# Optimization experiments

Hardware: AMD Instinct MI355X
Metric: run time of the kernel (lower is better)

## Reference

```python
import jax, jax.numpy as jnp
import numpy as np

N = 50000      # nodes
E = 800000     # edges
D_IN = 128     # raw feature dim
H = 96         # hidden_channels
K = 8          # experts
L = 4          # num_layers
C = 40         # classes


def setup_inputs() -> dict:
    key = jax.random.key(0)
    ks = jax.random.split(key, 10)
    stdv = 1.0 / np.sqrt(H)
    inp = {
        'x': jax.random.normal(ks[0], (N, D_IN), dtype=jnp.float32),
        'edge_index': jax.random.randint(ks[1], (2, E), 0, N, dtype=jnp.int64),
        # fcs[0]: Linear(d, hidden); fcs[1]: Linear(hidden, c)
        'fc0_w': jax.random.normal(ks[2], (D_IN, H), dtype=jnp.float32) * 0.05,
        'fc0_b': jnp.zeros((H,), dtype=jnp.float32),
        'fc1_w': jax.random.normal(ks[3], (H, C), dtype=jnp.float32) * 0.05,
        'fc1_b': jnp.zeros((C,), dtype=jnp.float32),
        # context_enc (method='node'): per-layer Linear(hidden, K)
        'ctx_w': jax.random.normal(ks[4], (L, H, K), dtype=jnp.float32) * 0.05,
        'ctx_b': jnp.zeros((L, K), dtype=jnp.float32),
        # GraphMultiConvolution weights: [L, K, hidden, hidden], uniform(-stdv, stdv)
        'conv_w': jax.random.uniform(ks[5], (L, K, H, H), dtype=jnp.float32,
                                     minval=-stdv, maxval=stdv),
    }
    return inp


def reference(x, edge_index, fc0_w, fc0_b, fc1_w, fc1_b, ctx_w, ctx_b, conv_w):
    # eval-mode forward (training=False): no dropout, softmax routing
    row = edge_index[0]
    col = edge_index[1]
    h = jax.nn.relu(x @ fc0_w + fc0_b)                     # [N, H]
    for i in range(L):
        # routing logits and soft expert weights z: [N, K]
        z = jax.nn.softmax(h @ ctx_w[i] + ctx_b[i], axis=-1)
        # spmm aggregation: hi[r] = sum over edges (r, c) of h[c]
        hi = jax.ops.segment_sum(h[col], row, num_segments=N)  # [N, H]
        # K-expert batched matmul: [N, K, H]
        outs = jnp.einsum('nd,kdo->nko', hi, conv_w[i])
        # gumbel/softmax-weighted combine + residual
        out = jnp.einsum('nk,nko->no', z, outs) + h
        h = jax.nn.relu(out)
    return h @ fc1_w + fc1_b                               # [N, C]
```

## Files before the change

kernel.cpp:

```cpp
#include <hip/hip_runtime.h>

#define N_NODES 50000
#define N_EDGES 800000
#define DIN     128
#define H       96
#define K_EXP   8
#define L_LAYERS 4
#define C_OUT   40

#define GSZ 6250

typedef _Float16 f16;
typedef f16 f16x2 __attribute__((ext_vector_type(2)));
typedef f16 f16x4 __attribute__((ext_vector_type(4)));
typedef f16 f16x8 __attribute__((ext_vector_type(8)));
typedef float f32x4 __attribute__((ext_vector_type(4)));

#define CONV_TOT (L_LAYERS * K_EXP * H * H)
#define FC0_TOT  (DIN * H)
#define FC1_TOT  (48 * H)


__global__ __launch_bounds__(256) void count_convert(const int* __restrict__ row,
                                                     int* __restrict__ deg,
                                                     int* __restrict__ p,
                                                     const float* __restrict__ conv_w,
                                                     const float* __restrict__ fc0_w,
                                                     const float* __restrict__ fc1_w,
                                                     f16* __restrict__ wfrag,
                                                     f16* __restrict__ fc0t,
                                                     f16* __restrict__ fc1t) {
    int i = blockIdx.x * blockDim.x + threadIdx.x;
    if (i < N_EDGES) {
        p[i] = atomicAdd(&deg[row[i]], 1);
        return;
    }
    int j = i - N_EDGES;
    if (j < CONV_TOT) {
        int o = j % H;
        int t = j / H;
        int d = t % H;
        int lk = t / H;
        int ct = o >> 4, lc = o & 15;
        int ks = d >> 5, quad = (d >> 3) & 3, jj = d & 7;
        wfrag[(size_t)lk * 9216 + ct * 1536 + ks * 512 + (quad * 16 + lc) * 8 + jj] =
            (f16)conv_w[j];
    } else if (j < CONV_TOT + FC0_TOT) {
        int q = j - CONV_TOT;
        int o = q % H, d = q / H;
        fc0t[o * DIN + d] = (f16)fc0_w[q];
    } else if (j < CONV_TOT + FC0_TOT + FC1_TOT) {
        int q = j - CONV_TOT - FC0_TOT;
        int o = q / H, d = q % H;
        fc1t[q] = (o < C_OUT) ? (f16)fc1_w[d * C_OUT + o] : (f16)0.f;
    }
}

__global__ __launch_bounds__(1024) void scanA(const int* __restrict__ deg,
                                              int* __restrict__ rowptr,
                                              int* __restrict__ partial, int n) {
    __shared__ int wsum[16];
    int tid  = threadIdx.x;
    int lane = tid & 63, wid = tid >> 6;
    int idx = blockIdx.x * 1024 + tid;
    int v = (idx < n) ? deg[idx] : 0;
    int s = v;
    #pragma unroll
    for (int off = 1; off < 64; off <<= 1) {
        int t = __shfl_up(s, off, 64);
        if (lane >= off) s += t;
    }
    if (lane == 63) wsum[wid] = s;
    __syncthreads();
    if (wid == 0 && lane < 16) {
        int w = wsum[lane];
        #pragma unroll
        for (int off = 1; off < 16; off <<= 1) {
            int t = __shfl_up(w, off, 16);
            if (lane >= off) w += t;
        }
        wsum[lane] = w;
    }
    __syncthreads();
    int waveoff = (wid == 0) ? 0 : wsum[wid - 1];
    if (idx < n) rowptr[idx + 1] = waveoff + s;
    if (tid == 1023) partial[blockIdx.x] = waveoff + s;
}

__global__ __launch_bounds__(1024) void scanC(int* __restrict__ rowptr,
                                              const int* __restrict__ partial,
                                              int nb, int n) {
    __shared__ int boff_s;
    int tid = threadIdx.x;
    if (tid < 64) {
        int v = (tid < nb && tid < (int)blockIdx.x) ? partial[tid] : 0;
        #pragma unroll
        for (int off = 32; off >= 1; off >>= 1) v += __shfl_xor(v, off, 64);
        if (tid == 0) boff_s = v;
    }
    __syncthreads();
    int boff = boff_s;
    int idx = blockIdx.x * 1024 + tid;
    if (idx == 0) rowptr[0] = 0;
    if (idx < n) rowptr[idx + 1] += boff;
}

__global__ __launch_bounds__(256) void scatter_store_xcd(const int* __restrict__ row,
                                                         const int* __restrict__ col,
                                                         const int* __restrict__ p,
                                                         const int* __restrict__ rowptr,
                                                         int* __restrict__ csr, int e) {
    int g = blockIdx.x & 7;
    int rlo = g * GSZ, rhi = rlo + GSZ;
    int stride = (gridDim.x >> 3) * 256;
    for (int i = (blockIdx.x >> 3) * 256 + threadIdx.x; i < e; i += stride) {
        int r = row[i];
        if (r >= rlo && r < rhi)
            csr[rowptr[r] + p[i]] = col[i];
    }
}


#define SPMM_BLOCKS ((N_NODES + 31) / 32)
#define CTX_BLOCKS  ((N_NODES + 255) / 256)

__global__ __launch_bounds__(256) void layer_pre(const f16* __restrict__ h16,
                                                 const int* __restrict__ rowptr,
                                                 const int* __restrict__ csr,
                                                 f16* __restrict__ hi16,
                                                 const float* __restrict__ cw,
                                                 const float* __restrict__ cb,
                                                 float* __restrict__ zt, int n) {
    __shared__ float ws[H * K_EXP];
    __shared__ float bs[K_EXP];
    int tid = threadIdx.x;
    if ((int)blockIdx.x < SPMM_BLOCKS) {
        int r0 = blockIdx.x * 32 + (tid >> 4);
        int r1 = r0 + 16;
        int li = tid & 15;
        if (r0 >= n) return;
        int j0 = rowptr[r0], e0 = rowptr[r0 + 1];
        int j1 = 0, e1 = 0;
        if (r1 < n) { j1 = rowptr[r1]; e1 = rowptr[r1 + 1]; }
        bool act = li < 12;
        float accA[8] = {}, accB[8] = {};
        for (;;) {
            int m0 = e0 - j0; if (m0 > 16) m0 = 16;
            int m1 = e1 - j1; if (m1 > 16) m1 = 16;
            if (m0 <= 0 && m1 <= 0) break;
            int c0 = 0, c1 = 0;
            if (li < m0) c0 = csr[j0 + li];
            if (li < m1) c1 = csr[j1 + li];
            int mm = m0 > m1 ? m0 : m1;
            int t = 0;
            for (; t + 4 <= mm; t += 4) {
                f16x8 vA[4], vB[4];
                bool aA[4], aB[4];
                #pragma unroll
                for (int u = 0; u < 4; u++) {
                    int cc0 = __shfl(c0, t + u, 16);
                    int cc1 = __shfl(c1, t + u, 16);
                    aA[u] = act && (t + u < m0);
                    aB[u] = act && (t + u < m1);
                    vA[u] = f16x8{}; vB[u] = f16x8{};
                    if (aA[u]) vA[u] = *(const f16x8*)(h16 + (size_t)cc0 * H + li * 8);
                    if (aB[u]) vB[u] = *(const f16x8*)(h16 + (size_t)cc1 * H + li * 8);
                }
                #pragma unroll
                for (int u = 0; u < 4; u++) {
                    if (aA[u]) {
                        #pragma unroll
                        for (int q = 0; q < 8; q++) accA[q] += (float)vA[u][q];
                    }
                    if (aB[u]) {
                        #pragma unroll
                        for (int q = 0; q < 8; q++) accB[q] += (float)vB[u][q];
                    }
                }
            }
            for (; t < mm; t++) {
                int cc0 = __shfl(c0, t, 16), cc1 = __shfl(c1, t, 16);
                bool a0 = act && (t < m0), a1 = act && (t < m1);
                f16x8 v0 = {}, v1 = {};
                if (a0) v0 = *(const f16x8*)(h16 + (size_t)cc0 * H + li * 8);
                if (a1) v1 = *(const f16x8*)(h16 + (size_t)cc1 * H + li * 8);
                if (a0) {
                    #pragma unroll
                    for (int q = 0; q < 8; q++) accA[q] += (float)v0[q];
                }
                if (a1) {
                    #pragma unroll
                    for (int q = 0; q < 8; q++) accB[q] += (float)v1[q];
                }
            }
            j0 += m0; j1 += m1;
        }
        if (act) {
            f16x8 oA;
            #pragma unroll
            for (int q = 0; q < 8; q++) oA[q] = (f16)accA[q];
            *(f16x8*)(hi16 + (size_t)r0 * H + li * 8) = oA;
            if (r1 < n) {
                f16x8 oB;
                #pragma unroll
                for (int q = 0; q < 8; q++) oB[q] = (f16)accB[q];
                *(f16x8*)(hi16 + (size_t)r1 * H + li * 8) = oB;
            }
        }
    } else {
        for (int t = tid; t < H * K_EXP; t += 256) ws[t] = cw[t];
        if (tid < K_EXP) bs[tid] = cb[tid];
        __syncthreads();
        int node = ((int)blockIdx.x - SPMM_BLOCKS) * 256 + tid;
        if (node >= n) return;
        float acc[K_EXP];
        #pragma unroll
        for (int k = 0; k < K_EXP; k++) acc[k] = bs[k];
        const f16* hr = h16 + (size_t)node * H;
        #pragma unroll 3
        for (int c8 = 0; c8 < 12; c8++) {
            f16x8 v = *(const f16x8*)(hr + c8 * 8);
            #pragma unroll
            for (int j = 0; j < 8; j++) {
                float hv = (float)v[j];
                int d = c8 * 8 + j;
                #pragma unroll
                for (int k = 0; k < K_EXP; k++) acc[k] += hv * ws[d * K_EXP + k];
            }
        }
        float mx = acc[0];
        #pragma unroll
        for (int k = 1; k < K_EXP; k++) mx = fmaxf(mx, acc[k]);
        float s = 0.f;
        #pragma unroll
        for (int k = 0; k < K_EXP; k++) { acc[k] = __expf(acc[k] - mx); s += acc[k]; }
        float inv = 1.f / s;
        #pragma unroll
        for (int k = 0; k < K_EXP; k++)
            zt[(size_t)k * N_NODES + node] = acc[k] * inv;
    }
}


#define FPAD 136

__global__ __launch_bounds__(256) void fc0_kernel(const float* __restrict__ x,
                                                  const f16* __restrict__ fc0t,
                                                  const float* __restrict__ b,
                                                  f16* __restrict__ h16, int n) {
    __shared__ f16 As[64 * FPAD];
    __shared__ f16 Ws[96 * FPAD];
    int tid = threadIdx.x;
    int l = tid & 63, w = tid >> 6;
    int quad = l >> 4, lc = l & 15;
    int row0 = blockIdx.x * 64;

    for (int t = tid; t < 2048; t += 256) {
        int m = t >> 5, c4 = (t & 31) * 4;
        int gr = row0 + m;
        float4 v = {0.f, 0.f, 0.f, 0.f};
        if (gr < n) v = *(const float4*)(x + (size_t)gr * DIN + c4);
        f16x4 h4 = {(f16)v.x, (f16)v.y, (f16)v.z, (f16)v.w};
        *(f16x4*)&As[m * FPAD + c4] = h4;
    }
    for (int t = tid; t < 1536; t += 256) {
        int o = t >> 4, c8 = (t & 15) * 8;
        *(f16x8*)&Ws[o * FPAD + c8] = *(const f16x8*)(fc0t + o * DIN + c8);
    }
    __syncthreads();

    f16x8 afr[4];
    #pragma unroll
    for (int ks = 0; ks < 4; ks++)
        afr[ks] = *(const f16x8*)&As[(16 * w + lc) * FPAD + ks * 32 + quad * 8];

    f32x4 acc[6] = {};
    #pragma unroll
    for (int ct = 0; ct < 6; ct++) {
        #pragma unroll
        for (int ks = 0; ks < 4; ks++) {
            f16x8 bfr = *(const f16x8*)&Ws[(ct * 16 + lc) * FPAD + ks * 32 + quad * 8];
            acc[ct] = __builtin_amdgcn_mfma_f32_16x16x32_f16(afr[ks], bfr, acc[ct], 0, 0, 0);
        }
    }

    int m0 = 16 * w + quad * 4;
    #pragma unroll
    for (int r = 0; r < 4; r++) {
        int gr = row0 + m0 + r;
        if (gr < n) {
            #pragma unroll
            for (int ct = 0; ct < 6; ct++) {
                int o = ct * 16 + lc;
                h16[(size_t)gr * H + o] = (f16)fmaxf(acc[ct][r] + b[o], 0.f);
            }
        }
    }
}


#define EG_STAGE 2
#define EG_HALFS (EG_STAGE * 9216)

__global__ __launch_bounds__(256) void expert_gemm(const f16* __restrict__ hi16,
                                                   const f16* __restrict__ hin16,
                                                   const f16* __restrict__ wfrag,
                                                   const float* __restrict__ zt,
                                                   f16* __restrict__ hout16, int n) {
    __shared__ f16 Wl[EG_HALFS];
    int tid = threadIdx.x;
    int l = tid & 63, w = tid >> 6;
    int quad = l >> 4, lc = l & 15;
    int wrow0 = blockIdx.x * 64 + w * 16;

    f16x8 afr[3];
    #pragma unroll
    for (int ks = 0; ks < 3; ks++)
        afr[ks] = *(const f16x8*)(hi16 + (size_t)(wrow0 + lc) * H + ks * 32 + quad * 8);

    f32x4 acc[6] = {};

    for (int kb = 0; kb < K_EXP; kb += EG_STAGE) {
        __syncthreads();
        const f16* src = wfrag + (size_t)kb * 9216;
        for (int t = tid; t < EG_HALFS / 8; t += 256)
            *(f16x8*)&Wl[t * 8] = *(const f16x8*)(src + t * 8);
        __syncthreads();

        #pragma unroll
        for (int k2 = 0; k2 < EG_STAGE; k2++) {
            int k = kb + k2;
            f32x4 zf = *(const f32x4*)(zt + (size_t)k * N_NODES + wrow0 + quad * 4);
            #pragma unroll
            for (int ct = 0; ct < 6; ct++) {
                f16x8 b0 = *(const f16x8*)&Wl[k2 * 9216 + ct * 1536 + 0 * 512 + l * 8];
                f16x8 b1 = *(const f16x8*)&Wl[k2 * 9216 + ct * 1536 + 1 * 512 + l * 8];
                f16x8 b2 = *(const f16x8*)&Wl[k2 * 9216 + ct * 1536 + 2 * 512 + l * 8];
                f32x4 tmp = {};
                tmp = __builtin_amdgcn_mfma_f32_16x16x32_f16(afr[0], b0, tmp, 0, 0, 0);
                tmp = __builtin_amdgcn_mfma_f32_16x16x32_f16(afr[1], b1, tmp, 0, 0, 0);
                tmp = __builtin_amdgcn_mfma_f32_16x16x32_f16(afr[2], b2, tmp, 0, 0, 0);
                acc[ct] += zf * tmp;
            }
        }
    }

    #pragma unroll
    for (int r = 0; r < 4; r++) {
        int gr = wrow0 + quad * 4 + r;
        if (gr < n) {
            #pragma unroll
            for (int ct = 0; ct < 6; ct++) {
                int o = ct * 16 + lc;
                float v = fmaxf(acc[ct][r] + (float)hin16[(size_t)gr * H + o], 0.f);
                hout16[(size_t)gr * H + o] = (f16)v;
            }
        }
    }
}


#define APAD 104

__global__ __launch_bounds__(256) void fc1_kernel(const f16* __restrict__ h16,
                                                  const f16* __restrict__ fc1t,
                                                  const float* __restrict__ b,
                                                  float* __restrict__ out, int n) {
    __shared__ f16 As[64 * APAD];
    __shared__ f16 Ws[48 * APAD];
    int tid = threadIdx.x;
    int l = tid & 63, w = tid >> 6;
    int quad = l >> 4, lc = l & 15;
    int row0 = blockIdx.x * 64;

    for (int t = tid; t < 768; t += 256) {
        int m = t / 12, c8 = (t % 12) * 8;
        int gr = row0 + m;
        f16x8 v = {};
        if (gr < n) v = *(const f16x8*)(h16 + (size_t)gr * H + c8);
        *(f16x8*)&As[m * APAD + c8] = v;
    }
    for (int t = tid; t < 576; t += 256) {
        int o = t / 12, c8 = (t % 12) * 8;
        *(f16x8*)&Ws[o * APAD + c8] = *(const f16x8*)(fc1t + o * H + c8);
    }
    __syncthreads();

    f16x8 afr[3];
    #pragma unroll
    for (int ks = 0; ks < 3; ks++)
        afr[ks] = *(const f16x8*)&As[(16 * w + lc) * APAD + ks * 32 + quad * 8];

    f32x4 acc[3] = {};
    #pragma unroll
    for (int ct = 0; ct < 3; ct++) {
        #pragma unroll
        for (int ks = 0; ks < 3; ks++) {
            f16x8 bfr = *(const f16x8*)&Ws[(ct * 16 + lc) * APAD + ks * 32 + quad * 8];
            acc[ct] = __builtin_amdgcn_mfma_f32_16x16x32_f16(afr[ks], bfr, acc[ct], 0, 0, 0);
        }
    }

    int m0 = 16 * w + quad * 4;
    #pragma unroll
    for (int r = 0; r < 4; r++) {
        int gr = row0 + m0 + r;
        if (gr < n) {
            #pragma unroll
            for (int ct = 0; ct < 3; ct++) {
                int o = ct * 16 + lc;
                if (o < C_OUT)
                    out[(size_t)gr * C_OUT + o] = acc[ct][r] + b[o];
            }
        }
    }
}


extern "C" void kernel_launch(void* const* d_in, const int* in_sizes, int n_in,
                              void* d_out, int out_size, void* d_ws, size_t ws_size,
                              hipStream_t stream) {
    const float* x      = (const float*)d_in[0];
    const int*   ei     = (const int*)d_in[1];
    const float* fc0_w  = (const float*)d_in[2];
    const float* fc0_b  = (const float*)d_in[3];
    const float* fc1_w  = (const float*)d_in[4];
    const float* fc1_b  = (const float*)d_in[5];
    const float* ctx_w  = (const float*)d_in[6];
    const float* ctx_b  = (const float*)d_in[7];
    const float* conv_w = (const float*)d_in[8];
    float* out = (float*)d_out;

    const size_t NH = (size_t)N_NODES * H;

    float* zbuf = (float*)d_ws;
    f16*   h16a = (f16*)(zbuf + (size_t)N_NODES * K_EXP);
    f16*   h16b = h16a + NH;
    f16*   hi16 = h16b + NH;
    f16*   wfrag= hi16 + NH;
    f16*   fc0t = wfrag + CONV_TOT;
    f16*   fc1t = fc0t + FC0_TOT;
    int* rowptr = (int*)(fc1t + FC1_TOT);
    int* deg    = rowptr + (N_NODES + 1);
    int* csr    = deg + N_NODES;
    int* prank  = csr + N_EDGES;
    int* partial  = prank + N_EDGES;

    const int* row = ei;
    const int* col = ei + N_EDGES;

    hipMemsetAsync(deg, 0, sizeof(int) * N_NODES, stream);

    int cc_total = N_EDGES + CONV_TOT + FC0_TOT + FC1_TOT;
    count_convert<<<(cc_total + 255) / 256, 256, 0, stream>>>(
        row, deg, prank, conv_w, fc0_w, fc1_w, wfrag, fc0t, fc1t);
    int nsb = (N_NODES + 1023) / 1024;
    scanA<<<nsb, 1024, 0, stream>>>(deg, rowptr, partial, N_NODES);
    scanC<<<nsb, 1024, 0, stream>>>(rowptr, partial, nsb, N_NODES);
    scatter_store_xcd<<<1024, 256, 0, stream>>>(row, col, prank, rowptr, csr, N_EDGES);

    int gemm_grid = (N_NODES + 63) / 64;
    fc0_kernel<<<gemm_grid, 256, 0, stream>>>(x, fc0t, fc0_b, h16a, N_NODES);

    f16* hcur = h16a;
    f16* hnext = h16b;
    for (int i = 0; i < L_LAYERS; i++) {
        layer_pre<<<SPMM_BLOCKS + CTX_BLOCKS, 256, 0, stream>>>(
            hcur, rowptr, csr, hi16,
            ctx_w + (size_t)i * H * K_EXP, ctx_b + (size_t)i * K_EXP, zbuf, N_NODES);
        expert_gemm<<<gemm_grid, 256, 0, stream>>>(
            hi16, hcur, wfrag + (size_t)i * K_EXP * H * H, zbuf, hnext, N_NODES);
        f16* t = hcur; hcur = hnext; hnext = t;
    }
    fc1_kernel<<<gemm_grid, 256, 0, stream>>>(hcur, fc1t, fc1_b, out, N_NODES);
}
```

Baseline: 385.5 us.

## Fuse SpMM, routing softmax and expert GEMM into one per-layer kernel

Merges the gather-aggregate, context softmax and K-expert MFMA GEMM into a single kernel per layer. Each 32-row block keeps its aggregated rows and routing weights in shared memory, so the hi16 and z buffers no longer round-trip through global memory and one launch per layer goes away. In exchange, each block now reloads all expert weights for only 32 rows instead of 64, which doubles weight staging traffic. The SpMM unroll also drops from 4 to 2, and the larger shared-memory footprint may limit occupancy.

```diff
diff --git a/kernel.cpp b/kernel.cpp
--- a/kernel.cpp
+++ b/kernel.cpp
@@ -121,26 +121,36 @@
 }
 
 
-#define SPMM_BLOCKS ((N_NODES + 31) / 32)
-#define CTX_BLOCKS  ((N_NODES + 255) / 256)
-
-__global__ __launch_bounds__(256) void layer_pre(const f16* __restrict__ h16,
-                                                 const int* __restrict__ rowptr,
-                                                 const int* __restrict__ csr,
-                                                 f16* __restrict__ hi16,
-                                                 const float* __restrict__ cw,
-                                                 const float* __restrict__ cb,
-                                                 float* __restrict__ zt, int n) {
+#define HSP 104
+#define EG_STAGE 2
+#define EG_HALFS (EG_STAGE * 9216)
+
+#define FUSED_BLOCKS ((N_NODES + 31) / 32)
+
+__global__ __launch_bounds__(256) void layer_fused(const f16* __restrict__ h16,
+                                                   const int* __restrict__ rowptr,
+                                                   const int* __restrict__ csr,
+                                                   const f16* __restrict__ wfrag,
+                                                   const float* __restrict__ cw,
+                                                   const float* __restrict__ cb,
+                                                   f16* __restrict__ hout16, int n) {
+    __shared__ f16 Hs[32 * HSP];
+    __shared__ float Zl[K_EXP * 32];
     __shared__ float ws[H * K_EXP];
     __shared__ float bs[K_EXP];
+    __shared__ f16 Wl[EG_HALFS];
+
     int tid = threadIdx.x;
-    if ((int)blockIdx.x < SPMM_BLOCKS) {
-        int r0 = blockIdx.x * 32 + (tid >> 4);
-        int r1 = r0 + 16;
-        int li = tid & 15;
-        if (r0 >= n) return;
-        int j0 = rowptr[r0], e0 = rowptr[r0 + 1];
-        int j1 = 0, e1 = 0;
+    int row0 = blockIdx.x * 32;
+
+    for (int t = tid; t < H * K_EXP; t += 256) ws[t] = cw[t];
+    if (tid < K_EXP) bs[tid] = cb[tid];
+
+    {
+        int g = tid >> 4, li = tid & 15;
+        int r0 = row0 + g, r1 = r0 + 16;
+        int j0 = 0, e0 = 0, j1 = 0, e1 = 0;
+        if (r0 < n) { j0 = rowptr[r0]; e0 = rowptr[r0 + 1]; }
         if (r1 < n) { j1 = rowptr[r1]; e1 = rowptr[r1 + 1]; }
         bool act = li < 12;
         float accA[8] = {}, accB[8] = {};
@@ -153,32 +163,34 @@
             if (li < m1) c1 = csr[j1 + li];
             int mm = m0 > m1 ? m0 : m1;
             int t = 0;
-            for (; t + 4 <= mm; t += 4) {
-                f16x8 vA[4], vB[4];
-                bool aA[4], aB[4];
-                #pragma unroll
-                for (int u = 0; u < 4; u++) {
-                    int cc0 = __shfl(c0, t + u, 16);
-                    int cc1 = __shfl(c1, t + u, 16);
-                    aA[u] = act && (t + u < m0);
-                    aB[u] = act && (t + u < m1);
-                    vA[u] = f16x8{}; vB[u] = f16x8{};
-                    if (aA[u]) vA[u] = *(const f16x8*)(h16 + (size_t)cc0 * H + li * 8);
-                    if (aB[u]) vB[u] = *(const f16x8*)(h16 + (size_t)cc1 * H + li * 8);
-                }
-                #pragma unroll
-                for (int u = 0; u < 4; u++) {
-                    if (aA[u]) {
-                        #pragma unroll
-                        for (int q = 0; q < 8; q++) accA[q] += (float)vA[u][q];
-                    }
-                    if (aB[u]) {
-                        #pragma unroll
-                        for (int q = 0; q < 8; q++) accB[q] += (float)vB[u][q];
-                    }
-                }
-            }
-            for (; t < mm; t++) {
+            for (; t + 2 <= mm; t += 2) {
+                int cc0a = __shfl(c0, t, 16),     cc1a = __shfl(c1, t, 16);
+                int cc0b = __shfl(c0, t + 1, 16), cc1b = __shfl(c1, t + 1, 16);
+                bool a0a = act && (t < m0),     a1a = act && (t < m1);
+                bool a0b = act && (t + 1 < m0), a1b = act && (t + 1 < m1);
+                f16x8 v0a = {}, v1a = {}, v0b = {}, v1b = {};
+                if (a0a) v0a = *(const f16x8*)(h16 + (size_t)cc0a * H + li * 8);
+                if (a1a) v1a = *(const f16x8*)(h16 + (size_t)cc1a * H + li * 8);
+                if (a0b) v0b = *(const f16x8*)(h16 + (size_t)cc0b * H + li * 8);
+                if (a1b) v1b = *(const f16x8*)(h16 + (size_t)cc1b * H + li * 8);
+                if (a0a) {
+                    #pragma unroll
+                    for (int q = 0; q < 8; q++) accA[q] += (float)v0a[q];
+                }
+                if (a1a) {
+                    #pragma unroll
+                    for (int q = 0; q < 8; q++) accB[q] += (float)v1a[q];
+                }
+                if (a0b) {
+                    #pragma unroll
+                    for (int q = 0; q < 8; q++) accA[q] += (float)v0b[q];
+                }
+                if (a1b) {
+                    #pragma unroll
+                    for (int q = 0; q < 8; q++) accB[q] += (float)v1b[q];
+                }
+            }
+            if (t < mm) {
                 int cc0 = __shfl(c0, t, 16), cc1 = __shfl(c1, t, 16);
                 bool a0 = act && (t < m0), a1 = act && (t < m1);
                 f16x8 v0 = {}, v1 = {};
@@ -196,48 +208,87 @@
             j0 += m0; j1 += m1;
         }
         if (act) {
-            f16x8 oA;
-            #pragma unroll
-            for (int q = 0; q < 8; q++) oA[q] = (f16)accA[q];
-            *(f16x8*)(hi16 + (size_t)r0 * H + li * 8) = oA;
-            if (r1 < n) {
-                f16x8 oB;
-                #pragma unroll
-                for (int q = 0; q < 8; q++) oB[q] = (f16)accB[q];
-                *(f16x8*)(hi16 + (size_t)r1 * H + li * 8) = oB;
-            }
-        }
-    } else {
-        for (int t = tid; t < H * K_EXP; t += 256) ws[t] = cw[t];
-        if (tid < K_EXP) bs[tid] = cb[tid];
-        __syncthreads();
-        int node = ((int)blockIdx.x - SPMM_BLOCKS) * 256 + tid;
-        if (node >= n) return;
-        float acc[K_EXP];
-        #pragma unroll
-        for (int k = 0; k < K_EXP; k++) acc[k] = bs[k];
-        const f16* hr = h16 + (size_t)node * H;
+            f16x8 oA, oB;
+            #pragma unroll
+            for (int q = 0; q < 8; q++) { oA[q] = (f16)accA[q]; oB[q] = (f16)accB[q]; }
+            *(f16x8*)&Hs[g * HSP + li * 8] = oA;
+            *(f16x8*)&Hs[(g + 16) * HSP + li * 8] = oB;
+        }
+    }
+    __syncthreads();
+
+    {
+        int row8 = tid >> 3, k = tid & 7;
+        int gr = row0 + row8;
+        int grc = gr < n ? gr : 0;
+        const f16* hr = h16 + (size_t)grc * H;
+        float acc = bs[k];
         #pragma unroll 3
         for (int c8 = 0; c8 < 12; c8++) {
             f16x8 v = *(const f16x8*)(hr + c8 * 8);
             #pragma unroll
-            for (int j = 0; j < 8; j++) {
-                float hv = (float)v[j];
-                int d = c8 * 8 + j;
-                #pragma unroll
-                for (int k = 0; k < K_EXP; k++) acc[k] += hv * ws[d * K_EXP + k];
-            }
-        }
-        float mx = acc[0];
-        #pragma unroll
-        for (int k = 1; k < K_EXP; k++) mx = fmaxf(mx, acc[k]);
-        float s = 0.f;
-        #pragma unroll
-        for (int k = 0; k < K_EXP; k++) { acc[k] = __expf(acc[k] - mx); s += acc[k]; }
-        float inv = 1.f / s;
-        #pragma unroll
-        for (int k = 0; k < K_EXP; k++)
-            zt[(size_t)k * N_NODES + node] = acc[k] * inv;
+            for (int j = 0; j < 8; j++)
+                acc += (float)v[j] * ws[(c8 * 8 + j) * K_EXP + k];
+        }
+        float mx = acc;
+        #pragma unroll
+        for (int off = 4; off >= 1; off >>= 1) mx = fmaxf(mx, __shfl_xor(mx, off, 8));
+        float e = __expf(acc - mx);
+        float s = e;
+        #pragma unroll
+        for (int off = 4; off >= 1; off >>= 1) s += __shfl_xor(s, off, 8);
+        Zl[k * 32 + row8] = e / s;
+    }
+
+    int l = tid & 63, w = tid >> 6;
+    int quad = l >> 4, lc = l & 15;
+    int rt = w >> 1;
+    int ch = w & 1;
+
+    f16x8 afr[3];
+    #pragma unroll
+    for (int ks = 0; ks < 3; ks++)
+        afr[ks] = *(const f16x8*)&Hs[(rt * 16 + lc) * HSP + ks * 32 + quad * 8];
+
+    f32x4 acc3[3] = {};
+
+    for (int kb = 0; kb < K_EXP; kb += EG_STAGE) {
+        __syncthreads();
+        const f16* src = wfrag + (size_t)kb * 9216;
+        for (int t = tid; t < EG_HALFS / 8; t += 256)
+            *(f16x8*)&Wl[t * 8] = *(const f16x8*)(src + t * 8);
+        __syncthreads();
+
+        #pragma unroll
+        for (int k2 = 0; k2 < EG_STAGE; k2++) {
+            int k = kb + k2;
+            f32x4 zf = *(const f32x4*)&Zl[k * 32 + rt * 16 + quad * 4];
+            #pragma unroll
+            for (int ct = 0; ct < 3; ct++) {
+                int cti = ch * 3 + ct;
+                f16x8 b0 = *(const f16x8*)&Wl[k2 * 9216 + cti * 1536 + 0 * 512 + l * 8];
+                f16x8 b1 = *(const f16x8*)&Wl[k2 * 9216 + cti * 1536 + 1 * 512 + l * 8];
+                f16x8 b2 = *(const f16x8*)&Wl[k2 * 9216 + cti * 1536 + 2 * 512 + l * 8];
+                f32x4 tmp = {};
+                tmp = __builtin_amdgcn_mfma_f32_16x16x32_f16(afr[0], b0, tmp, 0, 0, 0);
+                tmp = __builtin_amdgcn_mfma_f32_16x16x32_f16(afr[1], b1, tmp, 0, 0, 0);
+                tmp = __builtin_amdgcn_mfma_f32_16x16x32_f16(afr[2], b2, tmp, 0, 0, 0);
+                acc3[ct] += zf * tmp;
+            }
+        }
+    }
+
+    #pragma unroll
+    for (int r = 0; r < 4; r++) {
+        int gr = row0 + rt * 16 + quad * 4 + r;
+        if (gr < n) {
+            #pragma unroll
+            for (int ct = 0; ct < 3; ct++) {
+                int o = (ch * 3 + ct) * 16 + lc;
+                float v = fmaxf(acc3[ct][r] + (float)h16[(size_t)gr * H + o], 0.f);
+                hout16[(size_t)gr * H + o] = (f16)v;
+            }
+        }
     }
 }
 
@@ -293,67 +344,6 @@
             for (int ct = 0; ct < 6; ct++) {
                 int o = ct * 16 + lc;
                 h16[(size_t)gr * H + o] = (f16)fmaxf(acc[ct][r] + b[o], 0.f);
-            }
-        }
-    }
-}
-
-
-#define EG_STAGE 2
-#define EG_HALFS (EG_STAGE * 9216)
-
-__global__ __launch_bounds__(256) void expert_gemm(const f16* __restrict__ hi16,
-                                                   const f16* __restrict__ hin16,
-                                                   const f16* __restrict__ wfrag,
-                                                   const float* __restrict__ zt,
-                                                   f16* __restrict__ hout16, int n) {
-    __shared__ f16 Wl[EG_HALFS];
-    int tid = threadIdx.x;
-    int l = tid & 63, w = tid >> 6;
-    int quad = l >> 4, lc = l & 15;
-    int wrow0 = blockIdx.x * 64 + w * 16;
-
-    f16x8 afr[3];
-    #pragma unroll
-    for (int ks = 0; ks < 3; ks++)
-        afr[ks] = *(const f16x8*)(hi16 + (size_t)(wrow0 + lc) * H + ks * 32 + quad * 8);
-
-    f32x4 acc[6] = {};
-
-    for (int kb = 0; kb < K_EXP; kb += EG_STAGE) {
-        __syncthreads();
-        const f16* src = wfrag + (size_t)kb * 9216;
-        for (int t = tid; t < EG_HALFS / 8; t += 256)
-            *(f16x8*)&Wl[t * 8] = *(const f16x8*)(src + t * 8);
-        __syncthreads();
-
-        #pragma unroll
-        for (int k2 = 0; k2 < EG_STAGE; k2++) {
-            int k = kb + k2;
-            f32x4 zf = *(const f32x4*)(zt + (size_t)k * N_NODES + wrow0 + quad * 4);
-            #pragma unroll
-            for (int ct = 0; ct < 6; ct++) {
-                f16x8 b0 = *(const f16x8*)&Wl[k2 * 9216 + ct * 1536 + 0 * 512 + l * 8];
-                f16x8 b1 = *(const f16x8*)&Wl[k2 * 9216 + ct * 1536 + 1 * 512 + l * 8];
-                f16x8 b2 = *(const f16x8*)&Wl[k2 * 9216 + ct * 1536 + 2 * 512 + l * 8];
-                f32x4 tmp = {};
-                tmp = __builtin_amdgcn_mfma_f32_16x16x32_f16(afr[0], b0, tmp, 0, 0, 0);
-                tmp = __builtin_amdgcn_mfma_f32_16x16x32_f16(afr[1], b1, tmp, 0, 0, 0);
-                tmp = __builtin_amdgcn_mfma_f32_16x16x32_f16(afr[2], b2, tmp, 0, 0, 0);
-                acc[ct] += zf * tmp;
-            }
-        }
-    }
-
-    #pragma unroll
-    for (int r = 0; r < 4; r++) {
-        int gr = wrow0 + quad * 4 + r;
-        if (gr < n) {
-            #pragma unroll
-            for (int ct = 0; ct < 6; ct++) {
-                int o = ct * 16 + lc;
-                float v = fmaxf(acc[ct][r] + (float)hin16[(size_t)gr * H + o], 0.f);
-                hout16[(size_t)gr * H + o] = (f16)v;
             }
         }
     }
@@ -433,11 +423,9 @@
 
     const size_t NH = (size_t)N_NODES * H;
 
-    float* zbuf = (float*)d_ws;
-    f16*   h16a = (f16*)(zbuf + (size_t)N_NODES * K_EXP);
+    f16*   h16a = (f16*)d_ws;
     f16*   h16b = h16a + NH;
-    f16*   hi16 = h16b + NH;
-    f16*   wfrag= hi16 + NH;
+    f16*   wfrag= h16b + NH;
     f16*   fc0t = wfrag + CONV_TOT;
     f16*   fc1t = fc0t + FC0_TOT;
     int* rowptr = (int*)(fc1t + FC1_TOT);
@@ -465,11 +453,10 @@
     f16* hcur = h16a;
     f16* hnext = h16b;
     for (int i = 0; i < L_LAYERS; i++) {
-        layer_pre<<<SPMM_BLOCKS + CTX_BLOCKS, 256, 0, stream>>>(
-            hcur, rowptr, csr, hi16,
-            ctx_w + (size_t)i * H * K_EXP, ctx_b + (size_t)i * K_EXP, zbuf, N_NODES);
-        expert_gemm<<<gemm_grid, 256, 0, stream>>>(
-            hi16, hcur, wfrag + (size_t)i * K_EXP * H * H, zbuf, hnext, N_NODES);
+        layer_fused<<<FUSED_BLOCKS, 256, 0, stream>>>(
+            hcur, rowptr, csr, wfrag + (size_t)i * K_EXP * H * H,
+            ctx_w + (size_t)i * H * K_EXP, ctx_b + (size_t)i * K_EXP,
+            hnext, N_NODES);
         f16* t = hcur; hcur = hnext; hnext = t;
     }
     fc1_kernel<<<gemm_grid, 256, 0, stream>>>(hcur, fc1t, fc1_b, out, N_NODES);
```

Measured after the change: 450.1 us. 1.17x slower.
